# Optimization experiments

Hardware: AMD Instinct MI355X
Metric: run time of the kernel (lower is better)

## Reference

```python
import jax, jax.numpy as jnp
import numpy as np

HIDDEN = 1024
HEADS = 16
HEAD_DIM = HIDDEN // HEADS
EPS = 1e-5


def setup_inputs() -> dict:
    key = jax.random.key(0)
    ks = jax.random.split(key, 12)
    B, S, H = 2, 2048, HIDDEN
    s = 1.0 / np.sqrt(H)
    x = jax.random.normal(ks[0], (B, S, H), dtype=jnp.float32)
    Wq = jax.random.normal(ks[1], (H, H), dtype=jnp.float32) * s
    bq = jnp.zeros((H,), dtype=jnp.float32)
    Wk = jax.random.normal(ks[2], (H, H), dtype=jnp.float32) * s
    bk = jnp.zeros((H,), dtype=jnp.float32)
    Wv = jax.random.normal(ks[3], (H, H), dtype=jnp.float32) * s
    bv = jnp.zeros((H,), dtype=jnp.float32)
    Wg = jax.random.normal(ks[4], (2 * H, H), dtype=jnp.float32) * (1.0 / np.sqrt(2 * H))
    bg = jnp.zeros((H,), dtype=jnp.float32)
    gamma = jnp.ones((H,), dtype=jnp.float32)
    beta = jnp.zeros((H,), dtype=jnp.float32)
    return {"x": x, "Wq": Wq, "bq": bq, "Wk": Wk, "bk": bk, "Wv": Wv, "bv": bv,
            "Wg": Wg, "bg": bg, "gamma": gamma, "beta": beta}


def reference(x, Wq, bq, Wk, bk, Wv, bv, Wg, bg, gamma, beta):
    B, S, H = x.shape
    def heads(t):  # [B,S,H] -> [B,nH,S,hd]
        return t.reshape(B, S, HEADS, HEAD_DIM).transpose(0, 2, 1, 3)
    Q = heads(x @ Wq + bq)
    K = heads(x @ Wk + bk)
    V = heads(x @ Wv + bv)
    scores = jnp.einsum('bhqd,bhkd->bhqk', Q, K) / jnp.sqrt(jnp.float32(HEAD_DIM))
    flow = scores - scores.transpose(0, 1, 3, 2)  # antisymmetric
    w = jax.nn.softmax(flow, axis=-1)
    flowed = jnp.einsum('bhqk,bhkd->bhqd', w, V)
    flowed = flowed.transpose(0, 2, 1, 3).reshape(B, S, H)
    gate = jax.nn.sigmoid(jnp.concatenate([x, flowed], axis=-1) @ Wg + bg)
    y = x + gate * flowed
    mu = jnp.mean(y, axis=-1, keepdims=True)
    var = jnp.mean(jnp.square(y - mu), axis=-1, keepdims=True)
    return (y - mu) * jax.lax.rsqrt(var + EPS) * gamma + beta
```

## Files before the change

### kernel.cpp

```cpp
#include <hip/hip_runtime.h>
#include <hip/hip_bf16.h>

#define S_LEN 2048
#define NHEAD 16
#define HDIM 64
#define HID 1024

typedef __attribute__((ext_vector_type(8))) short bf16x8;
typedef __attribute__((ext_vector_type(4))) float f32x4;
typedef __attribute__((ext_vector_type(2))) unsigned int u32x2;

__device__ __forceinline__ unsigned short f2bf(float x) {
    unsigned int u = __builtin_bit_cast(unsigned int, x);
    u = (u + 0x7fffu + ((u >> 16) & 1u)) >> 16;
    return (unsigned short)u;
}
__device__ __forceinline__ float bf2f(unsigned short s) {
    unsigned int u = ((unsigned int)s) << 16;
    return __builtin_bit_cast(float, u);
}
__device__ __forceinline__ unsigned cvtpk_bf16(float lo, float hi) {
    unsigned r;
    asm("v_cvt_pk_bf16_f32 %0, %1, %2" : "=v"(r) : "v"(lo), "v"(hi));
    return r;
}
__device__ __forceinline__ void gload16(const short* g, short* l) {
    __builtin_amdgcn_global_load_lds(
        (const __attribute__((address_space(1))) unsigned int*)g,
        (__attribute__((address_space(3))) unsigned int*)l, 16, 0, 0);
}
__device__ __forceinline__ bf16x8 negbf8(bf16x8 v) {
    bf16x8 r;
    #pragma unroll
    for (int e = 0; e < 8; e++) r[e] = v[e] ^ (short)0x8000;
    return r;
}

#define QSCALE 0.1803368801111168f

__global__ void cvt_kernel(const float* __restrict__ src, short* __restrict__ dst, int n4) {
    int i = blockIdx.x * blockDim.x + threadIdx.x;
    if (i < n4) {
        float4 v = reinterpret_cast<const float4*>(src)[i];
        short4 o;
        o.x = (short)f2bf(v.x); o.y = (short)f2bf(v.y);
        o.z = (short)f2bf(v.z); o.w = (short)f2bf(v.w);
        reinterpret_cast<short4*>(dst)[i] = o;
    }
}

__global__ void transpose_bf16(const float* __restrict__ src, short* __restrict__ dst,
                               int R, int C) {
    __shared__ float tile[32][33];
    int bx = blockIdx.x * 32;
    int by = blockIdx.y * 32;
    int tx = threadIdx.x, ty = threadIdx.y;
    #pragma unroll
    for (int i = ty; i < 32; i += 8)
        tile[i][tx] = src[(size_t)(by + i) * C + bx + tx];
    __syncthreads();
    #pragma unroll
    for (int i = ty; i < 32; i += 8)
        dst[(size_t)(bx + i) * R + by + tx] = (short)f2bf(tile[tx][i]);
}

__global__ void vtrans_kernel(const short* __restrict__ Vb, short* __restrict__ VT) {
    __shared__ short tile[32][34];
    int s0 = blockIdx.x * 32;
    int dv0 = blockIdx.y * 32;
    int bh = blockIdx.z;
    int b = bh >> 4, h = bh & 15;
    int tx = threadIdx.x, ty = threadIdx.y;
    #pragma unroll
    for (int i = ty; i < 32; i += 8)
        tile[i][tx] = Vb[(size_t)(b * S_LEN + s0 + i) * HID + h * HDIM + dv0 + tx];
    __syncthreads();
    #pragma unroll
    for (int i = ty; i < 32; i += 8)
        VT[(size_t)(bh * HDIM + dv0 + i) * S_LEN + s0 + tx] = tile[tx][i];
}

__global__ __launch_bounds__(256, 2)
void gemm_qkv(const short* __restrict__ xb, const short* __restrict__ WT,
              const float* __restrict__ bq, const float* __restrict__ bk,
              const float* __restrict__ bv,
              short* __restrict__ Qb, short* __restrict__ Kb, short* __restrict__ Vb) {
    __shared__ short Al[128 * 32];
    __shared__ short Bl[128 * 32];
    int mb = blockIdx.x, nb = blockIdx.y;
    int tid = threadIdx.x;
    int wave = tid >> 6, lane = tid & 63;
    int wm = wave >> 1, wn = wave & 1;
    int lr = lane & 15, lg = lane >> 4;

    int r = tid >> 2;
    int c = tid & 3;
    int sc = (c ^ (r & 3)) * 8;
    int dst0 = tid * 8;
    int dst1 = (tid + 256) * 8;
    const short* a0 = xb + (size_t)(mb * 128 + r) * 1024 + sc;
    const short* a1 = a0 + (size_t)64 * 1024;
    const short* b0 = WT + (size_t)(nb * 128 + r) * 1024 + sc;
    const short* b1 = b0 + (size_t)64 * 1024;
    int fsw = (lg ^ (lr & 3)) * 8;

    f32x4 acc[4][4] = {};

    for (int ks = 0; ks < 32; ++ks) {
        __syncthreads();
        gload16(a0 + ks * 32, &Al[dst0]);
        gload16(a1 + ks * 32, &Al[dst1]);
        gload16(b0 + ks * 32, &Bl[dst0]);
        gload16(b1 + ks * 32, &Bl[dst1]);
        __syncthreads();
        bf16x8 af[4], bfr[4];
        #pragma unroll
        for (int t = 0; t < 4; t++)
            af[t] = *(bf16x8*)&Al[(wm * 64 + t * 16 + lr) * 32 + fsw];
        #pragma unroll
        for (int t = 0; t < 4; t++)
            bfr[t] = *(bf16x8*)&Bl[(wn * 64 + t * 16 + lr) * 32 + fsw];
        #pragma unroll
        for (int i = 0; i < 4; i++)
            #pragma unroll
            for (int jn = 0; jn < 4; jn++)
                acc[i][jn] = __builtin_amdgcn_mfma_f32_16x16x32_bf16(af[i], bfr[jn], acc[i][jn], 0, 0, 0);
    }

    #pragma unroll
    for (int jn = 0; jn < 4; jn++) {
        int n = nb * 128 + wn * 64 + jn * 16 + lr;
        int which = n >> 10;
        int n1 = n & 1023;
        const float* bias = (which == 0) ? bq : (which == 1) ? bk : bv;
        short* out = (which == 0) ? Qb : (which == 1) ? Kb : Vb;
        float scale = (which == 0) ? QSCALE : 1.0f;
        float bv_ = bias[n1];
        #pragma unroll
        for (int i = 0; i < 4; i++) {
            #pragma unroll
            for (int j = 0; j < 4; j++) {
                int mm = mb * 128 + wm * 64 + i * 16 + lg * 4 + j;
                out[(size_t)mm * 1024 + n1] = (short)f2bf((acc[i][jn][j] + bv_) * scale);
            }
        }
    }
}

__global__ __launch_bounds__(256, 4)
void attn_kernel(const short* __restrict__ Qb, const short* __restrict__ Kb,
                 const short* __restrict__ VT, short* __restrict__ Fb) {
    __shared__ short Kt[64 * 64];
    __shared__ short Qt[64 * 64];
    __shared__ short Vt[64 * 64];
    __shared__ short Pl[4][16 * 64];

    int bid = blockIdx.x;
    int qb = bid & 31;
    int bh = bid >> 5;
    int b = bh >> 4, h = bh & 15;
    int tid = threadIdx.x;
    int wave = tid >> 6, lane = tid & 63;
    int lr = lane & 15, lg = lane >> 4;

    size_t rowbase = ((size_t)(b * S_LEN + qb * 64 + wave * 16 + lr)) * HID + h * HDIM;
    bf16x8 Qf[2], Kf[2];
    #pragma unroll
    for (int cc = 0; cc < 2; cc++) {
        Qf[cc] = *(const bf16x8*)(Qb + rowbase + cc * 32 + lg * 8);
        Kf[cc] = *(const bf16x8*)(Kb + rowbase + cc * 32 + lg * 8);
    }

    int r0 = tid >> 3;
    int c = tid & 7;
    int swz = (c ^ (r0 & 7)) * 8;
    int dst0 = r0 * 64 + swz;
    int dst1 = (r0 + 32) * 64 + swz;
    const short* kp = Kb + (size_t)(b * S_LEN + r0) * HID + h * HDIM + c * 8;
    const short* qp = Qb + (size_t)(b * S_LEN + r0) * HID + h * HDIM + c * 8;
    const short* vp = VT + (size_t)bh * HDIM * S_LEN + (size_t)r0 * S_LEN + c * 8;

    f32x4 O[4] = {};
    float m = -1e30f, l = 0.f;

    for (int kt = 0; kt < 32; ++kt) {
        __syncthreads();
        *(bf16x8*)&Kt[dst0] = *(const bf16x8*)kp;
        *(bf16x8*)&Kt[dst1] = *(const bf16x8*)(kp + 32 * HID);
        *(bf16x8*)&Qt[dst0] = negbf8(*(const bf16x8*)qp);
        *(bf16x8*)&Qt[dst1] = negbf8(*(const bf16x8*)(qp + 32 * HID));
        *(bf16x8*)&Vt[dst0] = *(const bf16x8*)vp;
        *(bf16x8*)&Vt[dst1] = *(const bf16x8*)(vp + 32 * S_LEN);
        kp += 64 * HID; qp += 64 * HID; vp += 64;
        __syncthreads();

        f32x4 S[4] = {};
        __builtin_amdgcn_s_setprio(1);
        #pragma unroll
        for (int t = 0; t < 4; t++) {
            #pragma unroll
            for (int c2 = 0; c2 < 2; c2++) {
                int fo = (t * 16 + lr) * 64 + (((4 * c2 + lg) ^ (lr & 7)) * 8);
                bf16x8 kf = *(bf16x8*)&Kt[fo];
                bf16x8 nqf = *(bf16x8*)&Qt[fo];
                S[t] = __builtin_amdgcn_mfma_f32_16x16x32_bf16(kf, Qf[c2], S[t], 0, 0, 0);
                S[t] = __builtin_amdgcn_mfma_f32_16x16x32_bf16(nqf, Kf[c2], S[t], 0, 0, 0);
            }
        }
        __builtin_amdgcn_s_setprio(0);

        float pm = -1e30f;
        #pragma unroll
        for (int t = 0; t < 4; t++)
            #pragma unroll
            for (int j = 0; j < 4; j++) pm = fmaxf(pm, S[t][j]);
        pm = fmaxf(pm, __shfl_xor(pm, 16));
        pm = fmaxf(pm, __shfl_xor(pm, 32));

        if (__any(pm > m + 8.f)) {
            float mn = fmaxf(m, pm);
            float alpha = exp2f(m - mn);
            m = mn;
            l *= alpha;
            float a[4];
            #pragma unroll
            for (int j = 0; j < 4; j++) a[j] = __shfl(alpha, lg * 4 + j);
            #pragma unroll
            for (int dvt = 0; dvt < 4; dvt++)
                #pragma unroll
                for (int j = 0; j < 4; j++) O[dvt][j] *= a[j];
        }

        float rs = 0.f;
        #pragma unroll
        for (int t = 0; t < 4; t++) {
            float p0 = exp2f(S[t][0] - m);
            float p1 = exp2f(S[t][1] - m);
            float p2 = exp2f(S[t][2] - m);
            float p3 = exp2f(S[t][3] - m);
            rs += (p0 + p1) + (p2 + p3);
            u32x2 pw;
            pw[0] = cvtpk_bf16(p0, p1);
            pw[1] = cvtpk_bf16(p2, p3);
            int po = lr * 64 + (((2 * t + (lg >> 1)) ^ (lr & 7)) * 8) + (lg & 1) * 4;
            *(u32x2*)&Pl[wave][po] = pw;
        }
        rs += __shfl_xor(rs, 16);
        rs += __shfl_xor(rs, 32);
        l += rs;

        __builtin_amdgcn_s_setprio(1);
        #pragma unroll
        for (int c2 = 0; c2 < 2; c2++) {
            bf16x8 pf = *(bf16x8*)&Pl[wave][lr * 64 + (((4 * c2 + lg) ^ (lr & 7)) * 8)];
            #pragma unroll
            for (int dvt = 0; dvt < 4; dvt++) {
                bf16x8 vf = *(bf16x8*)&Vt[(dvt * 16 + lr) * 64 + (((4 * c2 + lg) ^ (lr & 7)) * 8)];
                O[dvt] = __builtin_amdgcn_mfma_f32_16x16x32_bf16(pf, vf, O[dvt], 0, 0, 0);
            }
        }
        __builtin_amdgcn_s_setprio(0);
    }

    float linv = 1.f / l;
    float li[4];
    #pragma unroll
    for (int j = 0; j < 4; j++) li[j] = __shfl(linv, lg * 4 + j);
    #pragma unroll
    for (int dvt = 0; dvt < 4; dvt++) {
        #pragma unroll
        for (int j = 0; j < 4; j++) {
            int q = qb * 64 + wave * 16 + lg * 4 + j;
            int dv = dvt * 16 + lr;
            Fb[((size_t)(b * S_LEN + q)) * HID + h * HDIM + dv] =
                (short)f2bf(O[dvt][j] * li[j]);
        }
    }
}

__global__ __launch_bounds__(256, 2)
void gemm_gate(const short* __restrict__ xb, const short* __restrict__ fb,
               const short* __restrict__ WgT, const float* __restrict__ bg,
               const float* __restrict__ x, float* __restrict__ y) {
    __shared__ short Al[128 * 32];
    __shared__ short Bl[128 * 32];
    int mb = blockIdx.x, nb = blockIdx.y;
    int tid = threadIdx.x;
    int wave = tid >> 6, lane = tid & 63;
    int wm = wave >> 1, wn = wave & 1;
    int lr = lane & 15, lg = lane >> 4;

    int r = tid >> 2;
    int c = tid & 3;
    int sc = (c ^ (r & 3)) * 8;
    int dst0 = tid * 8;
    int dst1 = (tid + 256) * 8;
    size_t arow0 = (size_t)(mb * 128 + r) * 1024 + sc;
    size_t arow1 = arow0 + (size_t)64 * 1024;
    const short* b0 = WgT + (size_t)(nb * 128 + r) * 2048 + sc;
    const short* b1 = b0 + (size_t)64 * 2048;
    int fsw = (lg ^ (lr & 3)) * 8;

    f32x4 acc[4][4] = {};

    for (int ks = 0; ks < 64; ++ks) {
        int kg = ks * 32;
        const short* A = (kg < 1024) ? (xb + kg) : (fb + (kg - 1024));
        __syncthreads();
        gload16(A + arow0, &Al[dst0]);
        gload16(A + arow1, &Al[dst1]);
        gload16(b0 + kg, &Bl[dst0]);
        gload16(b1 + kg, &Bl[dst1]);
        __syncthreads();
        bf16x8 af[4], bfr[4];
        #pragma unroll
        for (int t = 0; t < 4; t++)
            af[t] = *(bf16x8*)&Al[(wm * 64 + t * 16 + lr) * 32 + fsw];
        #pragma unroll
        for (int t = 0; t < 4; t++)
            bfr[t] = *(bf16x8*)&Bl[(wn * 64 + t * 16 + lr) * 32 + fsw];
        #pragma unroll
        for (int i = 0; i < 4; i++)
            #pragma unroll
            for (int jn = 0; jn < 4; jn++)
                acc[i][jn] = __builtin_amdgcn_mfma_f32_16x16x32_bf16(af[i], bfr[jn], acc[i][jn], 0, 0, 0);
    }

    #pragma unroll
    for (int jn = 0; jn < 4; jn++) {
        int n = nb * 128 + wn * 64 + jn * 16 + lr;
        float bgv = bg[n];
        #pragma unroll
        for (int i = 0; i < 4; i++) {
            #pragma unroll
            for (int j = 0; j < 4; j++) {
                int mm = mb * 128 + wm * 64 + i * 16 + lg * 4 + j;
                size_t idx = (size_t)mm * 1024 + n;
                float z = acc[i][jn][j] + bgv;
                float gate = 1.f / (1.f + __expf(-z));
                float fv = bf2f((unsigned short)fb[idx]);
                y[idx] = x[idx] + gate * fv;
            }
        }
    }
}

__global__ __launch_bounds__(256)
void ln_kernel(float* __restrict__ y, const float* __restrict__ gamma,
               const float* __restrict__ beta) {
    int row = blockIdx.x;
    int tid = threadIdx.x;
    float4 v4 = *(const float4*)&y[(size_t)row * 1024 + tid * 4];
    float v[4] = {v4.x, v4.y, v4.z, v4.w};
    float s = v[0] + v[1] + v[2] + v[3];
    float s2 = v[0]*v[0] + v[1]*v[1] + v[2]*v[2] + v[3]*v[3];
    #pragma unroll
    for (int off = 1; off < 64; off <<= 1) {
        s += __shfl_xor(s, off);
        s2 += __shfl_xor(s2, off);
    }
    __shared__ float red[8];
    int wave = tid >> 6, lane = tid & 63;
    if (lane == 0) { red[wave] = s; red[4 + wave] = s2; }
    __syncthreads();
    s = red[0] + red[1] + red[2] + red[3];
    s2 = red[4] + red[5] + red[6] + red[7];
    float mu = s * (1.f / 1024.f);
    float var = s2 * (1.f / 1024.f) - mu * mu;
    float rsq = rsqrtf(var + 1e-5f);
    float4 o4;
    float* o = (float*)&o4;
    #pragma unroll
    for (int e = 0; e < 4; e++) {
        int n = tid * 4 + e;
        o[e] = (v[e] - mu) * rsq * gamma[n] + beta[n];
    }
    *(float4*)&y[(size_t)row * 1024 + tid * 4] = o4;
}

extern "C" void kernel_launch(void* const* d_in, const int* in_sizes, int n_in,
                              void* d_out, int out_size, void* d_ws, size_t ws_size,
                              hipStream_t stream) {
    const float* x     = (const float*)d_in[0];
    const float* Wq    = (const float*)d_in[1];
    const float* bq    = (const float*)d_in[2];
    const float* Wk    = (const float*)d_in[3];
    const float* bk    = (const float*)d_in[4];
    const float* Wv    = (const float*)d_in[5];
    const float* bv    = (const float*)d_in[6];
    const float* Wg    = (const float*)d_in[7];
    const float* bg    = (const float*)d_in[8];
    const float* gamma = (const float*)d_in[9];
    const float* beta  = (const float*)d_in[10];
    float* out = (float*)d_out;

    char* w = (char*)d_ws;
    const size_t MB = 1024 * 1024;
    short* xb  = (short*)(w + 0 * MB);
    short* Qb  = (short*)(w + 8 * MB);
    short* Kb  = (short*)(w + 16 * MB);
    short* Vb  = (short*)(w + 24 * MB);
    short* WT  = (short*)(w + 32 * MB);
    short* WgT = (short*)(w + 38 * MB);
    short* fb  = (short*)(w + 42 * MB);
    short* VT  = (short*)(w + 50 * MB);

    cvt_kernel<<<4096, 256, 0, stream>>>(x, xb, 4096 * 1024 / 4);
    dim3 tb(32, 8);
    transpose_bf16<<<dim3(32, 32), tb, 0, stream>>>(Wq, WT, 1024, 1024);
    transpose_bf16<<<dim3(32, 32), tb, 0, stream>>>(Wk, WT + 1024 * 1024, 1024, 1024);
    transpose_bf16<<<dim3(32, 32), tb, 0, stream>>>(Wv, WT + 2 * 1024 * 1024, 1024, 1024);
    transpose_bf16<<<dim3(32, 64), tb, 0, stream>>>(Wg, WgT, 2048, 1024);
    gemm_qkv<<<dim3(32, 24), 256, 0, stream>>>(xb, WT, bq, bk, bv, Qb, Kb, Vb);
    vtrans_kernel<<<dim3(64, 2, 32), tb, 0, stream>>>(Vb, VT);
    attn_kernel<<<1024, 256, 0, stream>>>(Qb, Kb, VT, fb);
    gemm_gate<<<dim3(32, 8), 256, 0, stream>>>(xb, fb, WgT, bg, x, out);
    ln_kernel<<<4096, 256, 0, stream>>>(out, gamma, beta);
}
```

Measured before the change: 208.1 us.

## Process 128 queries per attention block and load tiles directly into LDS

Each attention block now covers 128 query rows instead of 64, with every wave keeping two independent online-softmax states. This halves the K/Q/V tile traffic and LDS staging per query. Tile loads switch to global_load_lds with a pre-swizzled source address, skipping the register round trip. The sign flip moves from the Q tile in LDS to the per-wave K register fragments, so it happens once rather than on every tile. The cost is half as many blocks (512) and higher register pressure, which may reduce occupancy and latency hiding.

```diff
diff --git a/kernel.cpp b/kernel.cpp
--- a/kernel.cpp
+++ b/kernel.cpp
@@ -8,6 +8,7 @@
 
 typedef __attribute__((ext_vector_type(8))) short bf16x8;
 typedef __attribute__((ext_vector_type(4))) float f32x4;
+typedef __attribute__((ext_vector_type(4))) unsigned int u32x4;
 typedef __attribute__((ext_vector_type(2))) unsigned int u32x2;
 
 __device__ __forceinline__ unsigned short f2bf(float x) {
@@ -30,10 +31,10 @@
         (__attribute__((address_space(3))) unsigned int*)l, 16, 0, 0);
 }
 __device__ __forceinline__ bf16x8 negbf8(bf16x8 v) {
-    bf16x8 r;
-    #pragma unroll
-    for (int e = 0; e < 8; e++) r[e] = v[e] ^ (short)0x8000;
-    return r;
+    u32x4 u = __builtin_bit_cast(u32x4, v);
+    #pragma unroll
+    for (int e = 0; e < 4; e++) u[e] ^= 0x80008000u;
+    return __builtin_bit_cast(bf16x8, u);
 }
 
 #define QSCALE 0.1803368801111168f
@@ -153,48 +154,51 @@
     __shared__ short Kt[64 * 64];
     __shared__ short Qt[64 * 64];
     __shared__ short Vt[64 * 64];
-    __shared__ short Pl[4][16 * 64];
+    __shared__ short Pl[128 * 64];
 
     int bid = blockIdx.x;
-    int qb = bid & 31;
-    int bh = bid >> 5;
+    int qb = bid & 15;
+    int bh = bid >> 4;
     int b = bh >> 4, h = bh & 15;
     int tid = threadIdx.x;
     int wave = tid >> 6, lane = tid & 63;
     int lr = lane & 15, lg = lane >> 4;
 
-    size_t rowbase = ((size_t)(b * S_LEN + qb * 64 + wave * 16 + lr)) * HID + h * HDIM;
-    bf16x8 Qf[2], Kf[2];
-    #pragma unroll
-    for (int cc = 0; cc < 2; cc++) {
-        Qf[cc] = *(const bf16x8*)(Qb + rowbase + cc * 32 + lg * 8);
-        Kf[cc] = *(const bf16x8*)(Kb + rowbase + cc * 32 + lg * 8);
+    bf16x8 Qf[2][2], Kf[2][2];
+    #pragma unroll
+    for (int g = 0; g < 2; g++) {
+        size_t rowbase = ((size_t)(b * S_LEN + qb * 128 + g * 64 + wave * 16 + lr)) * HID + h * HDIM;
+        #pragma unroll
+        for (int cc = 0; cc < 2; cc++) {
+            Qf[g][cc] = *(const bf16x8*)(Qb + rowbase + cc * 32 + lg * 8);
+            Kf[g][cc] = negbf8(*(const bf16x8*)(Kb + rowbase + cc * 32 + lg * 8));
+        }
     }
 
     int r0 = tid >> 3;
     int c = tid & 7;
-    int swz = (c ^ (r0 & 7)) * 8;
-    int dst0 = r0 * 64 + swz;
-    int dst1 = (r0 + 32) * 64 + swz;
-    const short* kp = Kb + (size_t)(b * S_LEN + r0) * HID + h * HDIM + c * 8;
-    const short* qp = Qb + (size_t)(b * S_LEN + r0) * HID + h * HDIM + c * 8;
-    const short* vp = VT + (size_t)bh * HDIM * S_LEN + (size_t)r0 * S_LEN + c * 8;
-
-    f32x4 O[4] = {};
-    float m = -1e30f, l = 0.f;
+    int sc8 = (c ^ (r0 & 7)) * 8;
+    const short* kp = Kb + (size_t)(b * S_LEN + r0) * HID + h * HDIM + sc8;
+    const short* qp = Qb + (size_t)(b * S_LEN + r0) * HID + h * HDIM + sc8;
+    const short* vp = VT + (size_t)bh * HDIM * S_LEN + (size_t)r0 * S_LEN + sc8;
+    short* dK0 = &Kt[tid * 8]; short* dK1 = &Kt[(tid + 256) * 8];
+    short* dQ0 = &Qt[tid * 8]; short* dQ1 = &Qt[(tid + 256) * 8];
+    short* dV0 = &Vt[tid * 8]; short* dV1 = &Vt[(tid + 256) * 8];
+
+    f32x4 O0[4] = {}, O1[4] = {};
+    float m0 = -1e30f, l0 = 0.f, m1 = -1e30f, l1 = 0.f;
+    int prow0 = ((wave * 2 + 0) * 16 + lr) * 64;
+    int prow1 = ((wave * 2 + 1) * 16 + lr) * 64;
 
     for (int kt = 0; kt < 32; ++kt) {
         __syncthreads();
-        *(bf16x8*)&Kt[dst0] = *(const bf16x8*)kp;
-        *(bf16x8*)&Kt[dst1] = *(const bf16x8*)(kp + 32 * HID);
-        *(bf16x8*)&Qt[dst0] = negbf8(*(const bf16x8*)qp);
-        *(bf16x8*)&Qt[dst1] = negbf8(*(const bf16x8*)(qp + 32 * HID));
-        *(bf16x8*)&Vt[dst0] = *(const bf16x8*)vp;
-        *(bf16x8*)&Vt[dst1] = *(const bf16x8*)(vp + 32 * S_LEN);
+        gload16(kp, dK0); gload16(kp + 32 * HID, dK1);
+        gload16(qp, dQ0); gload16(qp + 32 * HID, dQ1);
+        gload16(vp, dV0); gload16(vp + 32 * S_LEN, dV1);
         kp += 64 * HID; qp += 64 * HID; vp += 64;
         __syncthreads();
 
-        f32x4 S[4] = {};
+        f32x4 S0[4] = {}, S1[4] = {};
         __builtin_amdgcn_s_setprio(1);
         #pragma unroll
         for (int t = 0; t < 4; t++) {
@@ -202,78 +206,109 @@
             for (int c2 = 0; c2 < 2; c2++) {
                 int fo = (t * 16 + lr) * 64 + (((4 * c2 + lg) ^ (lr & 7)) * 8);
                 bf16x8 kf = *(bf16x8*)&Kt[fo];
-                bf16x8 nqf = *(bf16x8*)&Qt[fo];
-                S[t] = __builtin_amdgcn_mfma_f32_16x16x32_bf16(kf, Qf[c2], S[t], 0, 0, 0);
-                S[t] = __builtin_amdgcn_mfma_f32_16x16x32_bf16(nqf, Kf[c2], S[t], 0, 0, 0);
+                bf16x8 qf = *(bf16x8*)&Qt[fo];
+                S0[t] = __builtin_amdgcn_mfma_f32_16x16x32_bf16(kf, Qf[0][c2], S0[t], 0, 0, 0);
+                S0[t] = __builtin_amdgcn_mfma_f32_16x16x32_bf16(qf, Kf[0][c2], S0[t], 0, 0, 0);
+                S1[t] = __builtin_amdgcn_mfma_f32_16x16x32_bf16(kf, Qf[1][c2], S1[t], 0, 0, 0);
+                S1[t] = __builtin_amdgcn_mfma_f32_16x16x32_bf16(qf, Kf[1][c2], S1[t], 0, 0, 0);
             }
         }
         __builtin_amdgcn_s_setprio(0);
 
-        float pm = -1e30f;
+        float pm0 = -1e30f, pm1 = -1e30f;
         #pragma unroll
         for (int t = 0; t < 4; t++)
             #pragma unroll
-            for (int j = 0; j < 4; j++) pm = fmaxf(pm, S[t][j]);
-        pm = fmaxf(pm, __shfl_xor(pm, 16));
-        pm = fmaxf(pm, __shfl_xor(pm, 32));
-
-        if (__any(pm > m + 8.f)) {
-            float mn = fmaxf(m, pm);
-            float alpha = exp2f(m - mn);
-            m = mn;
-            l *= alpha;
-            float a[4];
-            #pragma unroll
-            for (int j = 0; j < 4; j++) a[j] = __shfl(alpha, lg * 4 + j);
+            for (int j = 0; j < 4; j++) {
+                pm0 = fmaxf(pm0, S0[t][j]);
+                pm1 = fmaxf(pm1, S1[t][j]);
+            }
+        pm0 = fmaxf(pm0, __shfl_xor(pm0, 16));
+        pm0 = fmaxf(pm0, __shfl_xor(pm0, 32));
+        pm1 = fmaxf(pm1, __shfl_xor(pm1, 16));
+        pm1 = fmaxf(pm1, __shfl_xor(pm1, 32));
+
+        if (__any((pm0 > m0 + 8.f) || (pm1 > m1 + 8.f))) {
+            float mn0 = fmaxf(m0, pm0), mn1 = fmaxf(m1, pm1);
+            float al0 = exp2f(m0 - mn0), al1 = exp2f(m1 - mn1);
+            m0 = mn0; m1 = mn1;
+            l0 *= al0; l1 *= al1;
+            float a0[4], a1[4];
+            #pragma unroll
+            for (int j = 0; j < 4; j++) {
+                a0[j] = __shfl(al0, lg * 4 + j);
+                a1[j] = __shfl(al1, lg * 4 + j);
+            }
             #pragma unroll
             for (int dvt = 0; dvt < 4; dvt++)
                 #pragma unroll
-                for (int j = 0; j < 4; j++) O[dvt][j] *= a[j];
-        }
-
-        float rs = 0.f;
+                for (int j = 0; j < 4; j++) {
+                    O0[dvt][j] *= a0[j];
+                    O1[dvt][j] *= a1[j];
+                }
+        }
+
+        float rs0 = 0.f, rs1 = 0.f;
         #pragma unroll
         for (int t = 0; t < 4; t++) {
-            float p0 = exp2f(S[t][0] - m);
-            float p1 = exp2f(S[t][1] - m);
-            float p2 = exp2f(S[t][2] - m);
-            float p3 = exp2f(S[t][3] - m);
-            rs += (p0 + p1) + (p2 + p3);
+            float p0 = exp2f(S0[t][0] - m0), p1 = exp2f(S0[t][1] - m0);
+            float p2 = exp2f(S0[t][2] - m0), p3 = exp2f(S0[t][3] - m0);
+            rs0 += (p0 + p1) + (p2 + p3);
             u32x2 pw;
             pw[0] = cvtpk_bf16(p0, p1);
             pw[1] = cvtpk_bf16(p2, p3);
-            int po = lr * 64 + (((2 * t + (lg >> 1)) ^ (lr & 7)) * 8) + (lg & 1) * 4;
-            *(u32x2*)&Pl[wave][po] = pw;
-        }
-        rs += __shfl_xor(rs, 16);
-        rs += __shfl_xor(rs, 32);
-        l += rs;
+            int po = prow0 + (((2 * t + (lg >> 1)) ^ (lr & 7)) * 8) + (lg & 1) * 4;
+            *(u32x2*)&Pl[po] = pw;
+        }
+        #pragma unroll
+        for (int t = 0; t < 4; t++) {
+            float p0 = exp2f(S1[t][0] - m1), p1 = exp2f(S1[t][1] - m1);
+            float p2 = exp2f(S1[t][2] - m1), p3 = exp2f(S1[t][3] - m1);
+            rs1 += (p0 + p1) + (p2 + p3);
+            u32x2 pw;
+            pw[0] = cvtpk_bf16(p0, p1);
+            pw[1] = cvtpk_bf16(p2, p3);
+            int po = prow1 + (((2 * t + (lg >> 1)) ^ (lr & 7)) * 8) + (lg & 1) * 4;
+            *(u32x2*)&Pl[po] = pw;
+        }
+        rs0 += __shfl_xor(rs0, 16);
+        rs0 += __shfl_xor(rs0, 32);
+        rs1 += __shfl_xor(rs1, 16);
+        rs1 += __shfl_xor(rs1, 32);
+        l0 += rs0; l1 += rs1;
 
         __builtin_amdgcn_s_setprio(1);
         #pragma unroll
         for (int c2 = 0; c2 < 2; c2++) {
-            bf16x8 pf = *(bf16x8*)&Pl[wave][lr * 64 + (((4 * c2 + lg) ^ (lr & 7)) * 8)];
+            int pc = ((4 * c2 + lg) ^ (lr & 7)) * 8;
+            bf16x8 pf0 = *(bf16x8*)&Pl[prow0 + pc];
+            bf16x8 pf1 = *(bf16x8*)&Pl[prow1 + pc];
             #pragma unroll
             for (int dvt = 0; dvt < 4; dvt++) {
-                bf16x8 vf = *(bf16x8*)&Vt[(dvt * 16 + lr) * 64 + (((4 * c2 + lg) ^ (lr & 7)) * 8)];
-                O[dvt] = __builtin_amdgcn_mfma_f32_16x16x32_bf16(pf, vf, O[dvt], 0, 0, 0);
+                bf16x8 vf = *(bf16x8*)&Vt[(dvt * 16 + lr) * 64 + pc];
+                O0[dvt] = __builtin_amdgcn_mfma_f32_16x16x32_bf16(pf0, vf, O0[dvt], 0, 0, 0);
+                O1[dvt] = __builtin_amdgcn_mfma_f32_16x16x32_bf16(pf1, vf, O1[dvt], 0, 0, 0);
             }
         }
         __builtin_amdgcn_s_setprio(0);
     }
 
-    float linv = 1.f / l;
-    float li[4];
-    #pragma unroll
-    for (int j = 0; j < 4; j++) li[j] = __shfl(linv, lg * 4 + j);
+    float li0[4], li1[4];
+    float v0 = 1.f / l0, v1 = 1.f / l1;
+    #pragma unroll
+    for (int j = 0; j < 4; j++) {
+        li0[j] = __shfl(v0, lg * 4 + j);
+        li1[j] = __shfl(v1, lg * 4 + j);
+    }
     #pragma unroll
     for (int dvt = 0; dvt < 4; dvt++) {
         #pragma unroll
         for (int j = 0; j < 4; j++) {
-            int q = qb * 64 + wave * 16 + lg * 4 + j;
             int dv = dvt * 16 + lr;
-            Fb[((size_t)(b * S_LEN + q)) * HID + h * HDIM + dv] =
-                (short)f2bf(O[dvt][j] * li[j]);
+            int q0 = qb * 128 + wave * 16 + lg * 4 + j;
+            int q1 = q0 + 64;
+            Fb[((size_t)(b * S_LEN + q0)) * HID + h * HDIM + dv] = (short)f2bf(O0[dvt][j] * li0[j]);
+            Fb[((size_t)(b * S_LEN + q1)) * HID + h * HDIM + dv] = (short)f2bf(O1[dvt][j] * li1[j]);
         }
     }
 }
@@ -413,7 +448,7 @@
     transpose_bf16<<<dim3(32, 64), tb, 0, stream>>>(Wg, WgT, 2048, 1024);
     gemm_qkv<<<dim3(32, 24), 256, 0, stream>>>(xb, WT, bq, bk, bv, Qb, Kb, Vb);
     vtrans_kernel<<<dim3(64, 2, 32), tb, 0, stream>>>(Vb, VT);
-    attn_kernel<<<1024, 256, 0, stream>>>(Qb, Kb, VT, fb);
+    attn_kernel<<<512, 256, 0, stream>>>(Qb, Kb, VT, fb);
     gemm_gate<<<dim3(32, 8), 256, 0, stream>>>(xb, fb, WgT, bg, x, out);
     ln_kernel<<<4096, 256, 0, stream>>>(out, gamma, beta);
 }
```

Result: slower. 262.1 us (+25.9%).

## Rewrite attention with 32x32 MFMA, two waves per block, register-resident P

Applied to the files above, without the earlier changes.

The attention kernel moves from 4 waves using 16x16x32 MFMAs to 2 waves using 32x32x16 MFMAs, with each wave covering 32 query rows. The probability tile no longer round-trips through LDS: it is packed to bf16 and rearranged with cross-lane shuffles straight into the PV MFMA operand. Tile loads now use global_load_lds directly into swizzled LDS, and Q negation is folded into the per-wave K fragments. The aim is fewer LDS operations and larger MFMA tiles per instruction. The cost is fewer waves per block, higher register pressure and changed launch bounds, which could reduce latency hiding.

```diff
diff --git a/kernel.cpp b/kernel.cpp
--- a/kernel.cpp
+++ b/kernel.cpp
@@ -8,7 +8,8 @@
 
 typedef __attribute__((ext_vector_type(8))) short bf16x8;
 typedef __attribute__((ext_vector_type(4))) float f32x4;
-typedef __attribute__((ext_vector_type(2))) unsigned int u32x2;
+typedef __attribute__((ext_vector_type(16))) float f32x16;
+typedef __attribute__((ext_vector_type(4))) unsigned int u32x4;
 
 __device__ __forceinline__ unsigned short f2bf(float x) {
     unsigned int u = __builtin_bit_cast(unsigned int, x);
@@ -30,10 +31,10 @@
         (__attribute__((address_space(3))) unsigned int*)l, 16, 0, 0);
 }
 __device__ __forceinline__ bf16x8 negbf8(bf16x8 v) {
-    bf16x8 r;
-    #pragma unroll
-    for (int e = 0; e < 8; e++) r[e] = v[e] ^ (short)0x8000;
-    return r;
+    u32x4 u = __builtin_bit_cast(u32x4, v);
+    #pragma unroll
+    for (int e = 0; e < 4; e++) u[e] ^= 0x80008000u;
+    return __builtin_bit_cast(bf16x8, u);
 }
 
 #define QSCALE 0.1803368801111168f
@@ -147,134 +148,138 @@
     }
 }
 
-__global__ __launch_bounds__(256, 4)
+__global__ __launch_bounds__(128, 2)
 void attn_kernel(const short* __restrict__ Qb, const short* __restrict__ Kb,
                  const short* __restrict__ VT, short* __restrict__ Fb) {
     __shared__ short Kt[64 * 64];
     __shared__ short Qt[64 * 64];
     __shared__ short Vt[64 * 64];
-    __shared__ short Pl[4][16 * 64];
 
     int bid = blockIdx.x;
     int qb = bid & 31;
     int bh = bid >> 5;
     int b = bh >> 4, h = bh & 15;
     int tid = threadIdx.x;
-    int wave = tid >> 6, lane = tid & 63;
-    int lr = lane & 15, lg = lane >> 4;
-
-    size_t rowbase = ((size_t)(b * S_LEN + qb * 64 + wave * 16 + lr)) * HID + h * HDIM;
-    bf16x8 Qf[2], Kf[2];
-    #pragma unroll
-    for (int cc = 0; cc < 2; cc++) {
-        Qf[cc] = *(const bf16x8*)(Qb + rowbase + cc * 32 + lg * 8);
-        Kf[cc] = *(const bf16x8*)(Kb + rowbase + cc * 32 + lg * 8);
-    }
-
-    int r0 = tid >> 3;
-    int c = tid & 7;
-    int swz = (c ^ (r0 & 7)) * 8;
-    int dst0 = r0 * 64 + swz;
-    int dst1 = (r0 + 32) * 64 + swz;
-    const short* kp = Kb + (size_t)(b * S_LEN + r0) * HID + h * HDIM + c * 8;
-    const short* qp = Qb + (size_t)(b * S_LEN + r0) * HID + h * HDIM + c * 8;
-    const short* vp = VT + (size_t)bh * HDIM * S_LEN + (size_t)r0 * S_LEN + c * 8;
-
-    f32x4 O[4] = {};
-    float m = -1e30f, l = 0.f;
+    int w = tid >> 6, l = tid & 63;
+    int lq = l & 31, hi = l >> 5;
+
+    size_t qrow = (size_t)(b * S_LEN + qb * 64 + w * 32 + lq) * HID + h * HDIM;
+    bf16x8 Qf[4], nKf[4];
+    #pragma unroll
+    for (int s = 0; s < 4; s++) {
+        Qf[s]  = *(const bf16x8*)(Qb + qrow + s * 16 + hi * 8);
+        nKf[s] = negbf8(*(const bf16x8*)(Kb + qrow + s * 16 + hi * 8));
+    }
+
+    int roff[4], vroff[4], dsto[4];
+    #pragma unroll
+    for (int j = 0; j < 4; j++) {
+        int R = w * 4 + j;
+        int r = R * 8 + (l >> 3);
+        int c = l & 7;
+        int sw = (c ^ (r & 7)) * 8;
+        roff[j] = r * HID + sw;
+        vroff[j] = r * S_LEN + sw;
+        dsto[j] = R * 512 + l * 8;
+    }
+    const short* kbase = Kb + (size_t)b * S_LEN * HID + h * HDIM;
+    const short* qbase = Qb + (size_t)b * S_LEN * HID + h * HDIM;
+    const short* vbase = VT + (size_t)bh * HDIM * S_LEN;
+
+    f32x16 O0 = {}, O1 = {};
+    float m = -1e30f, lsum = 0.f;
 
     for (int kt = 0; kt < 32; ++kt) {
         __syncthreads();
-        *(bf16x8*)&Kt[dst0] = *(const bf16x8*)kp;
-        *(bf16x8*)&Kt[dst1] = *(const bf16x8*)(kp + 32 * HID);
-        *(bf16x8*)&Qt[dst0] = negbf8(*(const bf16x8*)qp);
-        *(bf16x8*)&Qt[dst1] = negbf8(*(const bf16x8*)(qp + 32 * HID));
-        *(bf16x8*)&Vt[dst0] = *(const bf16x8*)vp;
-        *(bf16x8*)&Vt[dst1] = *(const bf16x8*)(vp + 32 * S_LEN);
-        kp += 64 * HID; qp += 64 * HID; vp += 64;
-        __syncthreads();
-
-        f32x4 S[4] = {};
+        #pragma unroll
+        for (int j = 0; j < 4; j++) {
+            gload16(kbase + (size_t)kt * 64 * HID + roff[j], &Kt[dsto[j]]);
+            gload16(qbase + (size_t)kt * 64 * HID + roff[j], &Qt[dsto[j]]);
+            gload16(vbase + kt * 64 + vroff[j], &Vt[dsto[j]]);
+        }
+        __syncthreads();
+
+        f32x16 S0 = {}, S1 = {};
         __builtin_amdgcn_s_setprio(1);
         #pragma unroll
-        for (int t = 0; t < 4; t++) {
-            #pragma unroll
-            for (int c2 = 0; c2 < 2; c2++) {
-                int fo = (t * 16 + lr) * 64 + (((4 * c2 + lg) ^ (lr & 7)) * 8);
-                bf16x8 kf = *(bf16x8*)&Kt[fo];
-                bf16x8 nqf = *(bf16x8*)&Qt[fo];
-                S[t] = __builtin_amdgcn_mfma_f32_16x16x32_bf16(kf, Qf[c2], S[t], 0, 0, 0);
-                S[t] = __builtin_amdgcn_mfma_f32_16x16x32_bf16(nqf, Kf[c2], S[t], 0, 0, 0);
-            }
+        for (int s = 0; s < 4; s++) {
+            int ch = ((2 * s + hi) ^ (lq & 7)) * 8;
+            bf16x8 kf0 = *(bf16x8*)&Kt[lq * 64 + ch];
+            bf16x8 qf0 = *(bf16x8*)&Qt[lq * 64 + ch];
+            bf16x8 kf1 = *(bf16x8*)&Kt[(32 + lq) * 64 + ch];
+            bf16x8 qf1 = *(bf16x8*)&Qt[(32 + lq) * 64 + ch];
+            S0 = __builtin_amdgcn_mfma_f32_32x32x16_bf16(kf0, Qf[s], S0, 0, 0, 0);
+            S0 = __builtin_amdgcn_mfma_f32_32x32x16_bf16(qf0, nKf[s], S0, 0, 0, 0);
+            S1 = __builtin_amdgcn_mfma_f32_32x32x16_bf16(kf1, Qf[s], S1, 0, 0, 0);
+            S1 = __builtin_amdgcn_mfma_f32_32x32x16_bf16(qf1, nKf[s], S1, 0, 0, 0);
         }
         __builtin_amdgcn_s_setprio(0);
 
         float pm = -1e30f;
         #pragma unroll
-        for (int t = 0; t < 4; t++)
-            #pragma unroll
-            for (int j = 0; j < 4; j++) pm = fmaxf(pm, S[t][j]);
-        pm = fmaxf(pm, __shfl_xor(pm, 16));
+        for (int g = 0; g < 16; g++) pm = fmaxf(pm, fmaxf(S0[g], S1[g]));
         pm = fmaxf(pm, __shfl_xor(pm, 32));
 
         if (__any(pm > m + 8.f)) {
             float mn = fmaxf(m, pm);
-            float alpha = exp2f(m - mn);
-            m = mn;
-            l *= alpha;
-            float a[4];
+            float al = exp2f(m - mn);
+            m = mn; lsum *= al;
             #pragma unroll
-            for (int j = 0; j < 4; j++) a[j] = __shfl(alpha, lg * 4 + j);
-            #pragma unroll
-            for (int dvt = 0; dvt < 4; dvt++)
-                #pragma unroll
-                for (int j = 0; j < 4; j++) O[dvt][j] *= a[j];
-        }
-
+            for (int g = 0; g < 16; g++) {
+                float a = __shfl(al, (g & 3) + 8 * (g >> 2) + 4 * hi);
+                O0[g] *= a; O1[g] *= a;
+            }
+        }
+
+        unsigned pd0[8], pd1[8];
         float rs = 0.f;
         #pragma unroll
-        for (int t = 0; t < 4; t++) {
-            float p0 = exp2f(S[t][0] - m);
-            float p1 = exp2f(S[t][1] - m);
-            float p2 = exp2f(S[t][2] - m);
-            float p3 = exp2f(S[t][3] - m);
-            rs += (p0 + p1) + (p2 + p3);
-            u32x2 pw;
-            pw[0] = cvtpk_bf16(p0, p1);
-            pw[1] = cvtpk_bf16(p2, p3);
-            int po = lr * 64 + (((2 * t + (lg >> 1)) ^ (lr & 7)) * 8) + (lg & 1) * 4;
-            *(u32x2*)&Pl[wave][po] = pw;
-        }
-        rs += __shfl_xor(rs, 16);
+        for (int g = 0; g < 8; g++) {
+            float a0 = exp2f(S0[2 * g] - m), a1 = exp2f(S0[2 * g + 1] - m);
+            float b0 = exp2f(S1[2 * g] - m), b1 = exp2f(S1[2 * g + 1] - m);
+            rs += (a0 + a1) + (b0 + b1);
+            pd0[g] = cvtpk_bf16(a0, a1);
+            pd1[g] = cvtpk_bf16(b0, b1);
+        }
         rs += __shfl_xor(rs, 32);
-        l += rs;
+        lsum += rs;
 
         __builtin_amdgcn_s_setprio(1);
         #pragma unroll
-        for (int c2 = 0; c2 < 2; c2++) {
-            bf16x8 pf = *(bf16x8*)&Pl[wave][lr * 64 + (((4 * c2 + lg) ^ (lr & 7)) * 8)];
-            #pragma unroll
-            for (int dvt = 0; dvt < 4; dvt++) {
-                bf16x8 vf = *(bf16x8*)&Vt[(dvt * 16 + lr) * 64 + (((4 * c2 + lg) ^ (lr & 7)) * 8)];
-                O[dvt] = __builtin_amdgcn_mfma_f32_16x16x32_bf16(pf, vf, O[dvt], 0, 0, 0);
-            }
+        for (int ks = 0; ks < 4; ks++) {
+            int j0 = (ks & 1) * 4;
+            unsigned p0 = (ks < 2) ? pd0[j0 + 0] : pd1[j0 + 0];
+            unsigned p1 = (ks < 2) ? pd0[j0 + 1] : pd1[j0 + 1];
+            unsigned p2 = (ks < 2) ? pd0[j0 + 2] : pd1[j0 + 2];
+            unsigned p3 = (ks < 2) ? pd0[j0 + 3] : pd1[j0 + 3];
+            unsigned x0 = (unsigned)__shfl_xor((int)p0, 32);
+            unsigned x1 = (unsigned)__shfl_xor((int)p1, 32);
+            unsigned x2 = (unsigned)__shfl_xor((int)p2, 32);
+            unsigned x3 = (unsigned)__shfl_xor((int)p3, 32);
+            u32x4 fd;
+            fd[0] = hi ? x2 : p0;
+            fd[1] = hi ? x3 : p1;
+            fd[2] = hi ? p2 : x0;
+            fd[3] = hi ? p3 : x1;
+            bf16x8 pf = __builtin_bit_cast(bf16x8, fd);
+            int ch = ((2 * ks + hi) ^ (lq & 7)) * 8;
+            bf16x8 v0 = *(bf16x8*)&Vt[lq * 64 + ch];
+            bf16x8 v1 = *(bf16x8*)&Vt[(32 + lq) * 64 + ch];
+            O0 = __builtin_amdgcn_mfma_f32_32x32x16_bf16(pf, v0, O0, 0, 0, 0);
+            O1 = __builtin_amdgcn_mfma_f32_32x32x16_bf16(pf, v1, O1, 0, 0, 0);
         }
         __builtin_amdgcn_s_setprio(0);
     }
 
-    float linv = 1.f / l;
-    float li[4];
-    #pragma unroll
-    for (int j = 0; j < 4; j++) li[j] = __shfl(linv, lg * 4 + j);
-    #pragma unroll
-    for (int dvt = 0; dvt < 4; dvt++) {
-        #pragma unroll
-        for (int j = 0; j < 4; j++) {
-            int q = qb * 64 + wave * 16 + lg * 4 + j;
-            int dv = dvt * 16 + lr;
-            Fb[((size_t)(b * S_LEN + q)) * HID + h * HDIM + dv] =
-                (short)f2bf(O[dvt][j] * li[j]);
-        }
+    float linv = 1.f / lsum;
+    #pragma unroll
+    for (int g = 0; g < 16; g++) {
+        int ql = (g & 3) + 8 * (g >> 2) + 4 * hi;
+        float li = __shfl(linv, ql);
+        int qg = qb * 64 + w * 32 + ql;
+        size_t base = (size_t)(b * S_LEN + qg) * HID + h * HDIM;
+        Fb[base + lq]      = (short)f2bf(O0[g] * li);
+        Fb[base + 32 + lq] = (short)f2bf(O1[g] * li);
     }
 }
 
@@ -413,7 +418,7 @@
     transpose_bf16<<<dim3(32, 64), tb, 0, stream>>>(Wg, WgT, 2048, 1024);
     gemm_qkv<<<dim3(32, 24), 256, 0, stream>>>(xb, WT, bq, bk, bv, Qb, Kb, Vb);
     vtrans_kernel<<<dim3(64, 2, 32), tb, 0, stream>>>(Vb, VT);
-    attn_kernel<<<1024, 256, 0, stream>>>(Qb, Kb, VT, fb);
+    attn_kernel<<<1024, 128, 0, stream>>>(Qb, Kb, VT, fb);
     gemm_gate<<<dim3(32, 8), 256, 0, stream>>>(xb, fb, WgT, bg, x, out);
     ln_kernel<<<4096, 256, 0, stream>>>(out, gamma, beta);
 }
```

New measurement: 210.9 us. Within noise of the previous version (+1.3%).
